# Kernel optimization log

Measured on AMD Instinct MI355X. Metric: run time of the kernel, lower is better.

## Reference

```python
import jax, jax.numpy as jnp
import numpy as np

N = 100000   # num_nodes
E = 1600000  # num_edges
IN, HID, OUT = 128, 128, 64  # in_ft, 2*out_ft, out_ft


def setup_inputs() -> dict:
    key = jax.random.key(0)
    ks = jax.random.split(key, 8)
    x = jax.random.normal(ks[0], (N, IN), dtype=jnp.float32)
    edge_index = jax.random.randint(ks[1], (2, E), 0, N, dtype=jnp.int32)
    # Glorot-style init for GCNConv linear weights
    W1 = jax.random.normal(ks[2], (IN, HID), dtype=jnp.float32) / np.sqrt(IN).astype(np.float32)
    b1 = jnp.zeros((HID,), dtype=jnp.float32)
    W2 = jax.random.normal(ks[3], (HID, OUT), dtype=jnp.float32) / np.sqrt(HID).astype(np.float32)
    b2 = jnp.zeros((OUT,), dtype=jnp.float32)
    a = jnp.array([0.25], dtype=jnp.float32)  # shared PReLU slope (nn.PReLU default)
    return {"x": x, "edge_index": edge_index, "W1": W1, "b1": b1, "W2": W2, "b2": b2, "a": a}


def reference(x, edge_index, W1, b1, W2, b2, a):
    # PyG GCNConv semantics: add self-loops, symmetric normalization
    # norm_e = deg(src)^-1/2 * deg(dst)^-1/2, out[dst] += norm_e * (x @ W)[src] + bias
    src, dst = edge_index[0], edge_index[1]
    loops = jnp.arange(N, dtype=src.dtype)
    s = jnp.concatenate([src, loops])  # [E+N]
    d = jnp.concatenate([dst, loops])  # [E+N]
    deg = jax.ops.segment_sum(jnp.ones_like(d, dtype=x.dtype), d, num_segments=N)
    dis = jax.lax.rsqrt(deg)  # deg >= 1 thanks to self-loops
    norm = (dis[s] * dis[d])[:, None]  # [E+N, 1]

    def gcn_conv(h, W, b):
        hw = h @ W                                   # dense transform [N, F_out]
        msgs = hw[s] * norm                          # gather + scale  [E+N, F_out]
        return jax.ops.segment_sum(msgs, d, num_segments=N) + b  # scatter-add

    prelu = lambda v: jnp.where(v >= 0, v, a * v)

    h = prelu(gcn_conv(x, W1, b1))   # dropout p=0.0 -> identity
    return prelu(gcn_conv(h, W2, b2))
```

## Files before the change

### kernel.cpp

```cpp
#include <hip/hip_runtime.h>

#define N_NODES 100000
#define N_EDGES 1600000
#define BSH 9
#define NB  196
#define EPB 4096
#define CAPSH 14
#define GB  ((N_EDGES + EPB - 1) / EPB)
#define GG  ((N_NODES + 127) / 128)

typedef short bf16x8 __attribute__((ext_vector_type(8)));
typedef float f32x4 __attribute__((ext_vector_type(4)));
typedef float f32x2 __attribute__((ext_vector_type(2)));


__device__ __forceinline__ unsigned pack_bf16x2(float a, float b) {
    unsigned ua = __float_as_uint(a), ub = __float_as_uint(b);
    unsigned ra = (ua + 0x7fffu + ((ua >> 16) & 1u)) >> 16;
    unsigned rb = (ub + 0x7fffu + ((ub >> 16) & 1u)) >> 16;
    return ra | (rb << 16);
}
__device__ __forceinline__ unsigned short bf16_rne(float f) {
    unsigned u = __float_as_uint(f);
    return (unsigned short)((u + 0x7fffu + ((u >> 16) & 1u)) >> 16);
}
__device__ __forceinline__ f32x2 unpk(unsigned u) {
    f32x2 r;
    r.x = __uint_as_float(u << 16);
    r.y = __uint_as_float(u & 0xffff0000u);
    return r;
}


__device__ __forceinline__ void wt_body(const float* W, unsigned short* Wt, int C, int bid) {
    int t = bid * 256 + threadIdx.x;
    if (t >= 128 * C) return;
    int k = t / C, c = t % C;
    int g = k >> 3, j = k & 7;
    Wt[c * 128 + ((g ^ (c & 7)) << 3) + j] = bf16_rne(W[t]);
}

__global__ void setup_k(const float* __restrict__ W1, unsigned short* __restrict__ Wt1,
                        const float* __restrict__ W2, unsigned short* __restrict__ Wt2,
                        int* __restrict__ cursor) {
    int b = blockIdx.x;
    if (b < 64) { wt_body(W1, Wt1, 128, b); }
    else if (b < 96) { wt_body(W2, Wt2, 64, b - 64); }
    else {
        int t = threadIdx.x;
        if (t < NB) cursor[t] = t << CAPSH;
    }
}


__global__ __launch_bounds__(256) void bin_gemm1_k(
        const int* __restrict__ src, const int* __restrict__ dst,
        int* __restrict__ cursor, unsigned* __restrict__ binned,
        const float* __restrict__ X, const unsigned short* __restrict__ Wt,
        unsigned short* __restrict__ Y) {
    __shared__ int lhist[256];
    __shared__ int lcur[256];
    __shared__ short lds_w[128 * 128];
    int tid = threadIdx.x;

    if (blockIdx.x < GB) {
        lhist[tid] = 0;
        __syncthreads();
        int e0 = blockIdx.x * EPB;
#pragma unroll
        for (int i = 0; i < EPB / 256; ++i) {
            int e = e0 + i * 256 + tid;
            if (e < N_EDGES) atomicAdd(&lhist[dst[e] >> BSH], 1);
        }
        __syncthreads();
        {
            int c = lhist[tid];
            lcur[tid] = (tid < NB && c > 0) ? atomicAdd(&cursor[tid], c) : 0;
        }
        __syncthreads();
#pragma unroll
        for (int i = 0; i < EPB / 256; ++i) {
            int e = e0 + i * 256 + tid;
            if (e < N_EDGES) {
                int d = dst[e];
                int b = d >> BSH;
                int pos = atomicAdd(&lcur[b], 1);
                if (pos < ((b + 1) << CAPSH))
                    binned[pos] = ((unsigned)(d & ((1 << BSH) - 1)) << 17) | (unsigned)src[e];
            }
        }
        return;
    }

    {
        const uint4* srcp = (const uint4*)Wt;
        uint4* dstp = (uint4*)lds_w;
        for (int i = tid; i < 128 * 16; i += 256) dstp[i] = srcp[i];
    }
    __syncthreads();
    int lane = tid & 63;
    int r16 = lane & 15, kq = lane >> 4;
    int rbase = (blockIdx.x - GB) * 128 + (tid >> 6) * 32;
    f32x4 acc[2][8] = {};
#pragma unroll
    for (int kk = 0; kk < 4; ++kk) {
        int k0 = kk * 32 + kq * 8;
        bf16x8 a[2];
#pragma unroll
        for (int rt = 0; rt < 2; ++rt) {
            int row = rbase + rt * 16 + r16;
            if (row < N_NODES) {
                const float* xp = X + (size_t)row * 128 + k0;
                float4 f0 = *(const float4*)xp;
                float4 f1 = *(const float4*)(xp + 4);
                uint4 uu = make_uint4(pack_bf16x2(f0.x, f0.y), pack_bf16x2(f0.z, f0.w),
                                      pack_bf16x2(f1.x, f1.y), pack_bf16x2(f1.z, f1.w));
                a[rt] = *(bf16x8*)&uu;
            } else {
                bf16x8 z = {0, 0, 0, 0, 0, 0, 0, 0};
                a[rt] = z;
            }
        }
#pragma unroll
        for (int c = 0; c < 8; ++c) {
            int col = c * 16 + r16;
            int gp = (kk * 4 + kq) ^ (col & 7);
            bf16x8 b = *(const bf16x8*)&lds_w[col * 128 + gp * 8];
            acc[0][c] = __builtin_amdgcn_mfma_f32_16x16x32_bf16(a[0], b, acc[0][c], 0, 0, 0);
            acc[1][c] = __builtin_amdgcn_mfma_f32_16x16x32_bf16(a[1], b, acc[1][c], 0, 0, 0);
        }
    }
#pragma unroll
    for (int rt = 0; rt < 2; ++rt) {
#pragma unroll
        for (int c = 0; c < 8; ++c) {
#pragma unroll
            for (int r = 0; r < 4; ++r) {
                int row = rbase + rt * 16 + kq * 4 + r;
                if (row < N_NODES)
                    Y[(size_t)row * 128 + c * 16 + r16] = bf16_rne(acc[rt][c][r]);
            }
        }
    }
}


__global__ __launch_bounds__(256) void degcsr_k(const unsigned* __restrict__ binned,
                                                const int* __restrict__ cursor,
                                                int2* __restrict__ rowrange,
                                                float* __restrict__ dis,
                                                unsigned* __restrict__ edge, int n) {
    __shared__ int lcnt[1 << BSH];
    __shared__ int ls[256];
    int b = blockIdx.x, tid = threadIdx.x;
    for (int j = tid; j < (1 << BSH); j += 256) lcnt[j] = 0;
    __syncthreads();
    int base = b << CAPSH;
    int total = cursor[b] - base;
    for (int i = tid; i < total; i += 256)
        atomicAdd(&lcnt[binned[base + i] >> 17], 1);
    __syncthreads();
    int v0 = lcnt[2 * tid], v1 = lcnt[2 * tid + 1];
    int sv = v0 + v1;
    ls[tid] = sv;
    __syncthreads();
    for (int off = 1; off < 256; off <<= 1) {
        int t = 0;
        if (tid >= off) t = ls[tid - off];
        __syncthreads();
        ls[tid] += t;
        __syncthreads();
    }
    int pre = ls[tid] - sv;
    int start0 = base + pre;
    int start1 = start0 + v0;
    int nbase = b << BSH;
    int node0 = nbase + 2 * tid, node1 = node0 + 1;
    if (node0 < n) {
        rowrange[node0] = make_int2(start0, start0 + v0);
        dis[node0] = rsqrtf((float)(v0 + 1));
    }
    if (node1 < n) {
        rowrange[node1] = make_int2(start1, start1 + v1);
        dis[node1] = rsqrtf((float)(v1 + 1));
    }
    lcnt[2 * tid] = start0;
    lcnt[2 * tid + 1] = start1;
    __syncthreads();
    for (int i = tid; i < total; i += 256) {
        unsigned u = binned[base + i];
        int pos = atomicAdd(&lcnt[u >> 17], 1);
        edge[pos] = u & 0x1FFFFu;
    }
}


__global__ __launch_bounds__(256) void gemm2_k(const unsigned short* __restrict__ Xv,
                                               const unsigned short* __restrict__ Wt,
                                               unsigned short* __restrict__ Y, int nrows) {
    __shared__ short lds_w[64 * 128];
    int tid = threadIdx.x;
    {
        const uint4* srcp = (const uint4*)Wt;
        uint4* dstp = (uint4*)lds_w;
        for (int i = tid; i < 64 * 16; i += 256) dstp[i] = srcp[i];
    }
    __syncthreads();
    int lane = tid & 63;
    int r16 = lane & 15, kq = lane >> 4;
    int rbase = blockIdx.x * 128 + (tid >> 6) * 32;
    f32x4 acc[2][4] = {};
#pragma unroll
    for (int kk = 0; kk < 4; ++kk) {
        int k0 = kk * 32 + kq * 8;
        bf16x8 a[2];
#pragma unroll
        for (int rt = 0; rt < 2; ++rt) {
            int row = rbase + rt * 16 + r16;
            if (row < nrows) {
                a[rt] = *(const bf16x8*)(Xv + (size_t)row * 128 + k0);
            } else {
                bf16x8 z = {0, 0, 0, 0, 0, 0, 0, 0};
                a[rt] = z;
            }
        }
#pragma unroll
        for (int c = 0; c < 4; ++c) {
            int col = c * 16 + r16;
            int gp = (kk * 4 + kq) ^ (col & 7);
            bf16x8 b = *(const bf16x8*)&lds_w[col * 128 + gp * 8];
            acc[0][c] = __builtin_amdgcn_mfma_f32_16x16x32_bf16(a[0], b, acc[0][c], 0, 0, 0);
            acc[1][c] = __builtin_amdgcn_mfma_f32_16x16x32_bf16(a[1], b, acc[1][c], 0, 0, 0);
        }
    }
#pragma unroll
    for (int rt = 0; rt < 2; ++rt) {
#pragma unroll
        for (int c = 0; c < 4; ++c) {
#pragma unroll
            for (int r = 0; r < 4; ++r) {
                int row = rbase + rt * 16 + kq * 4 + r;
                if (row < nrows)
                    Y[(size_t)row * 64 + c * 16 + r16] = bf16_rne(acc[rt][c][r]);
            }
        }
    }
}


__global__ void agg1_k(const unsigned* __restrict__ hw, const int2* __restrict__ rowrange,
                       const unsigned* __restrict__ edge, const float* __restrict__ dis,
                       const float* __restrict__ bias, const float* __restrict__ aslope,
                       unsigned* __restrict__ out, int n) {
    int w = (blockIdx.x * 256 + threadIdx.x) >> 6;
    int lane = threadIdx.x & 63;
    int g = lane >> 4;
    unsigned li = lane & 15;
    int node = w * 4 + g;
    bool valid = node < n;
    int2 rr = valid ? rowrange[node] : make_int2(0, 0);
    int e0 = rr.x, e1 = rr.y;
    unsigned rowoff = li << 4;
    const char* hwb = (const char*)hw;
    f32x2 acc[4] = {};
    int e = e0;
    while (__any(e < e1)) {
        if (e < e1) {
            unsigned s[4];
            uint4 v[4];
            float wgt[4];
#pragma unroll
            for (int u = 0; u < 4; ++u) {
                int ee = e + u;
                unsigned ec = (unsigned)((ee < e1) ? ee : (e1 - 1));
                s[u] = edge[ec];
            }
#pragma unroll
            for (int u = 0; u < 4; ++u) {
                v[u] = *(const uint4*)(hwb + ((s[u] << 8) | rowoff));
                wgt[u] = dis[s[u]];
            }
#pragma unroll
            for (int u = 0; u < 4; ++u) {
                float nr = (e + u < e1) ? wgt[u] : 0.f;
                f32x2 nr2 = {nr, nr};
                acc[0] += unpk(v[u].x) * nr2;
                acc[1] += unpk(v[u].y) * nr2;
                acc[2] += unpk(v[u].z) * nr2;
                acc[3] += unpk(v[u].w) * nr2;
            }
        }
        e += 4;
    }
    if (valid) {
        float dn = dis[node];
        f32x2 dn2 = {dn, dn};
        uint4 v = *(const uint4*)(hwb + (((unsigned)node << 8) | rowoff));
        acc[0] += unpk(v.x) * dn2;
        acc[1] += unpk(v.y) * dn2;
        acc[2] += unpk(v.z) * dn2;
        acc[3] += unpk(v.w) * dn2;
        float4 b0 = ((const float4*)bias)[li * 2];
        float4 b1 = ((const float4*)bias)[li * 2 + 1];
        float al = aslope[0];
        float r[8] = {dn * acc[0].x + b0.x, dn * acc[0].y + b0.y,
                      dn * acc[1].x + b0.z, dn * acc[1].y + b0.w,
                      dn * acc[2].x + b1.x, dn * acc[2].y + b1.y,
                      dn * acc[3].x + b1.z, dn * acc[3].y + b1.w};
#pragma unroll
        for (int j = 0; j < 8; ++j) r[j] = (r[j] >= 0.f) ? r[j] : al * r[j];
        uint4 o = make_uint4(pack_bf16x2(r[0], r[1]), pack_bf16x2(r[2], r[3]),
                             pack_bf16x2(r[4], r[5]), pack_bf16x2(r[6], r[7]));
        *(uint4*)(out + (size_t)node * 64 + li * 4) = o;
    }
}

__global__ void agg2_k(const unsigned* __restrict__ hw, const int2* __restrict__ rowrange,
                       const unsigned* __restrict__ edge, const float* __restrict__ dis,
                       const float* __restrict__ bias, const float* __restrict__ aslope,
                       float* __restrict__ out, int n) {
    int w = (blockIdx.x * 256 + threadIdx.x) >> 6;
    int lane = threadIdx.x & 63;
    int g = lane >> 4;
    unsigned li = lane & 15;
    int node = w * 4 + g;
    bool valid = node < n;
    int2 rr = valid ? rowrange[node] : make_int2(0, 0);
    int e0 = rr.x, e1 = rr.y;
    unsigned rowoff = li << 3;
    const char* hwb = (const char*)hw;
    f32x2 acc[2] = {};
    int e = e0;
    while (__any(e < e1)) {
        if (e < e1) {
            unsigned s[8];
            uint2 v[8];
            float wgt[8];
#pragma unroll
            for (int u = 0; u < 8; ++u) {
                int ee = e + u;
                unsigned ec = (unsigned)((ee < e1) ? ee : (e1 - 1));
                s[u] = edge[ec];
            }
#pragma unroll
            for (int u = 0; u < 8; ++u) {
                v[u] = *(const uint2*)(hwb + ((s[u] << 7) | rowoff));
                wgt[u] = dis[s[u]];
            }
#pragma unroll
            for (int u = 0; u < 8; ++u) {
                float nr = (e + u < e1) ? wgt[u] : 0.f;
                f32x2 nr2 = {nr, nr};
                acc[0] += unpk(v[u].x) * nr2;
                acc[1] += unpk(v[u].y) * nr2;
            }
        }
        e += 8;
    }
    if (valid) {
        float dn = dis[node];
        f32x2 dn2 = {dn, dn};
        uint2 v = *(const uint2*)(hwb + (((unsigned)node << 7) | rowoff));
        acc[0] += unpk(v.x) * dn2;
        acc[1] += unpk(v.y) * dn2;
        float4 b = ((const float4*)bias)[li];
        float al = aslope[0];
        float r[4] = {dn * acc[0].x + b.x, dn * acc[0].y + b.y,
                      dn * acc[1].x + b.z, dn * acc[1].y + b.w};
#pragma unroll
        for (int j = 0; j < 4; ++j) r[j] = (r[j] >= 0.f) ? r[j] : al * r[j];
        *(float4*)(out + (size_t)node * 64 + li * 4) = make_float4(r[0], r[1], r[2], r[3]);
    }
}


extern "C" void kernel_launch(void* const* d_in, const int* in_sizes, int n_in,
                              void* d_out, int out_size, void* d_ws, size_t ws_size,
                              hipStream_t stream) {
    const float* x  = (const float*)d_in[0];
    const int*   ei = (const int*)d_in[1];
    const int*   src = ei;
    const int*   dst = ei + N_EDGES;
    const float* W1 = (const float*)d_in[2];
    const float* b1 = (const float*)d_in[3];
    const float* W2 = (const float*)d_in[4];
    const float* b2 = (const float*)d_in[5];
    const float* a  = (const float*)d_in[6];
    float* out = (float*)d_out;

    char* ws = (char*)d_ws;
    size_t off = 0;
    auto alloc = [&](size_t bytes) -> void* {
        void* p = ws + off;
        off += (bytes + 255) & ~(size_t)255;
        return p;
    };
    int2*           rowrange  = (int2*)alloc((size_t)N_NODES * 8);
    float*          dis       = (float*)alloc((size_t)N_NODES * 4);
    int*            cursor    = (int*)alloc(NB * 4);
    unsigned*       binned    = (unsigned*)alloc((size_t)NB * (1 << CAPSH) * 4);
    unsigned*       edge      = (unsigned*)alloc((size_t)NB * (1 << CAPSH) * 4);
    unsigned*       hw1       = (unsigned*)alloc((size_t)N_NODES * 64 * 4);
    unsigned*       hbuf      = (unsigned*)alloc((size_t)N_NODES * 64 * 4);
    unsigned*       hw2       = (unsigned*)alloc((size_t)N_NODES * 32 * 4);
    unsigned short* Wt1       = (unsigned short*)alloc(128 * 128 * 2);
    unsigned short* Wt2       = (unsigned short*)alloc(64 * 128 * 2);

    setup_k<<<97, 256, 0, stream>>>(W1, Wt1, W2, Wt2, cursor);
    bin_gemm1_k<<<GB + GG, 256, 0, stream>>>(src, dst, cursor, binned,
                                             x, Wt1, (unsigned short*)hw1);
    degcsr_k<<<NB, 256, 0, stream>>>(binned, cursor, rowrange, dis, edge, N_NODES);

    agg1_k<<<6250, 256, 0, stream>>>(hw1, rowrange, edge, dis, b1, a, hbuf, N_NODES);
    gemm2_k<<<GG, 256, 0, stream>>>((unsigned short*)hbuf, Wt2, (unsigned short*)hw2, N_NODES);
    agg2_k<<<6250, 256, 0, stream>>>(hw2, rowrange, edge, dis, b2, a, out, N_NODES);
}
```

Before: 174.3 us.

## Split aggregation feature columns into halves across paired blocks

Both aggregation kernels now split each node's feature row into two halves, each handled by a separate block, and double the grid. Blocks are interleaved in groups of 8 so that the two halves for the same node groups run close together, presumably so the halves share cached row lines and L2 locality is better. Each thread now gathers half as many bytes per edge, which exposes more parallelism and memory requests in flight. The cost is that the edge indices and dis weights are read twice, once per half.

Measured after the change: 198.8 us. 1.14x slower.

```diff
diff --git a/kernel.cpp b/kernel.cpp
--- a/kernel.cpp
+++ b/kernel.cpp
@@ -8,6 +8,8 @@
 #define CAPSH 14
 #define GB  ((N_EDGES + EPB - 1) / EPB)
 #define GG  ((N_NODES + 127) / 128)
+#define NGRP 6250
+#define AGRID (((NGRP + 3) / 4) * 8)
 
 typedef short bf16x8 __attribute__((ext_vector_type(8)));
 typedef float f32x4 __attribute__((ext_vector_type(4)));
@@ -252,82 +254,19 @@
                        const unsigned* __restrict__ edge, const float* __restrict__ dis,
                        const float* __restrict__ bias, const float* __restrict__ aslope,
                        unsigned* __restrict__ out, int n) {
-    int w = (blockIdx.x * 256 + threadIdx.x) >> 6;
-    int lane = threadIdx.x & 63;
+    int b = blockIdx.x;
+    unsigned half = (b & 7) >> 2;
+    int ng = (b >> 3) * 4 + (b & 3);
+    if (ng >= NGRP) return;
+    int tid = threadIdx.x;
+    int lane = tid & 63;
     int g = lane >> 4;
     unsigned li = lane & 15;
-    int node = w * 4 + g;
+    int node = ng * 16 + (tid >> 6) * 4 + g;
     bool valid = node < n;
     int2 rr = valid ? rowrange[node] : make_int2(0, 0);
     int e0 = rr.x, e1 = rr.y;
-    unsigned rowoff = li << 4;
-    const char* hwb = (const char*)hw;
-    f32x2 acc[4] = {};
-    int e = e0;
-    while (__any(e < e1)) {
-        if (e < e1) {
-            unsigned s[4];
-            uint4 v[4];
-            float wgt[4];
-#pragma unroll
-            for (int u = 0; u < 4; ++u) {
-                int ee = e + u;
-                unsigned ec = (unsigned)((ee < e1) ? ee : (e1 - 1));
-                s[u] = edge[ec];
-            }
-#pragma unroll
-            for (int u = 0; u < 4; ++u) {
-                v[u] = *(const uint4*)(hwb + ((s[u] << 8) | rowoff));
-                wgt[u] = dis[s[u]];
-            }
-#pragma unroll
-            for (int u = 0; u < 4; ++u) {
-                float nr = (e + u < e1) ? wgt[u] : 0.f;
-                f32x2 nr2 = {nr, nr};
-                acc[0] += unpk(v[u].x) * nr2;
-                acc[1] += unpk(v[u].y) * nr2;
-                acc[2] += unpk(v[u].z) * nr2;
-                acc[3] += unpk(v[u].w) * nr2;
-            }
-        }
-        e += 4;
-    }
-    if (valid) {
-        float dn = dis[node];
-        f32x2 dn2 = {dn, dn};
-        uint4 v = *(const uint4*)(hwb + (((unsigned)node << 8) | rowoff));
-        acc[0] += unpk(v.x) * dn2;
-        acc[1] += unpk(v.y) * dn2;
-        acc[2] += unpk(v.z) * dn2;
-        acc[3] += unpk(v.w) * dn2;
-        float4 b0 = ((const float4*)bias)[li * 2];
-        float4 b1 = ((const float4*)bias)[li * 2 + 1];
-        float al = aslope[0];
-        float r[8] = {dn * acc[0].x + b0.x, dn * acc[0].y + b0.y,
-                      dn * acc[1].x + b0.z, dn * acc[1].y + b0.w,
-                      dn * acc[2].x + b1.x, dn * acc[2].y + b1.y,
-                      dn * acc[3].x + b1.z, dn * acc[3].y + b1.w};
-#pragma unroll
-        for (int j = 0; j < 8; ++j) r[j] = (r[j] >= 0.f) ? r[j] : al * r[j];
-        uint4 o = make_uint4(pack_bf16x2(r[0], r[1]), pack_bf16x2(r[2], r[3]),
-                             pack_bf16x2(r[4], r[5]), pack_bf16x2(r[6], r[7]));
-        *(uint4*)(out + (size_t)node * 64 + li * 4) = o;
-    }
-}
-
-__global__ void agg2_k(const unsigned* __restrict__ hw, const int2* __restrict__ rowrange,
-                       const unsigned* __restrict__ edge, const float* __restrict__ dis,
-                       const float* __restrict__ bias, const float* __restrict__ aslope,
-                       float* __restrict__ out, int n) {
-    int w = (blockIdx.x * 256 + threadIdx.x) >> 6;
-    int lane = threadIdx.x & 63;
-    int g = lane >> 4;
-    unsigned li = lane & 15;
-    int node = w * 4 + g;
-    bool valid = node < n;
-    int2 rr = valid ? rowrange[node] : make_int2(0, 0);
-    int e0 = rr.x, e1 = rr.y;
-    unsigned rowoff = li << 3;
+    unsigned rowoff = (half << 7) | (li << 3);
     const char* hwb = (const char*)hw;
     f32x2 acc[2] = {};
     int e = e0;
@@ -344,7 +283,7 @@
             }
 #pragma unroll
             for (int u = 0; u < 8; ++u) {
-                v[u] = *(const uint2*)(hwb + ((s[u] << 7) | rowoff));
+                v[u] = *(const uint2*)(hwb + ((s[u] << 8) | rowoff));
                 wgt[u] = dis[s[u]];
             }
 #pragma unroll
@@ -360,16 +299,76 @@
     if (valid) {
         float dn = dis[node];
         f32x2 dn2 = {dn, dn};
-        uint2 v = *(const uint2*)(hwb + (((unsigned)node << 7) | rowoff));
+        uint2 v = *(const uint2*)(hwb + (((unsigned)node << 8) | rowoff));
         acc[0] += unpk(v.x) * dn2;
         acc[1] += unpk(v.y) * dn2;
-        float4 b = ((const float4*)bias)[li];
+        float4 bb = ((const float4*)bias)[half * 16 + li];
         float al = aslope[0];
-        float r[4] = {dn * acc[0].x + b.x, dn * acc[0].y + b.y,
-                      dn * acc[1].x + b.z, dn * acc[1].y + b.w};
+        float r[4] = {dn * acc[0].x + bb.x, dn * acc[0].y + bb.y,
+                      dn * acc[1].x + bb.z, dn * acc[1].y + bb.w};
 #pragma unroll
         for (int j = 0; j < 4; ++j) r[j] = (r[j] >= 0.f) ? r[j] : al * r[j];
-        *(float4*)(out + (size_t)node * 64 + li * 4) = make_float4(r[0], r[1], r[2], r[3]);
+        uint2 o = make_uint2(pack_bf16x2(r[0], r[1]), pack_bf16x2(r[2], r[3]));
+        *(uint2*)(out + (size_t)node * 64 + half * 32 + li * 2) = o;
+    }
+}
+
+__global__ void agg2_k(const unsigned* __restrict__ hw, const int2* __restrict__ rowrange,
+                       const unsigned* __restrict__ edge, const float* __restrict__ dis,
+                       const float* __restrict__ bias, const float* __restrict__ aslope,
+                       float* __restrict__ out, int n) {
+    int b = blockIdx.x;
+    unsigned half = (b & 7) >> 2;
+    int ng = (b >> 3) * 4 + (b & 3);
+    if (ng >= NGRP) return;
+    int tid = threadIdx.x;
+    int lane = tid & 63;
+    int g = lane >> 4;
+    unsigned li = lane & 15;
+    int node = ng * 16 + (tid >> 6) * 4 + g;
+    bool valid = node < n;
+    int2 rr = valid ? rowrange[node] : make_int2(0, 0);
+    int e0 = rr.x, e1 = rr.y;
+    unsigned rowoff = (half << 6) | (li << 2);
+    const char* hwb = (const char*)hw;
+    f32x2 acc = {};
+    int e = e0;
+    while (__any(e < e1)) {
+        if (e < e1) {
+            unsigned s[8];
+            unsigned v[8];
+            float wgt[8];
+#pragma unroll
+            for (int u = 0; u < 8; ++u) {
+                int ee = e + u;
+                unsigned ec = (unsigned)((ee < e1) ? ee : (e1 - 1));
+                s[u] = edge[ec];
+            }
+#pragma unroll
+            for (int u = 0; u < 8; ++u) {
+                v[u] = *(const unsigned*)(hwb + ((s[u] << 7) | rowoff));
+                wgt[u] = dis[s[u]];
+            }
+#pragma unroll
+            for (int u = 0; u < 8; ++u) {
+                float nr = (e + u < e1) ? wgt[u] : 0.f;
+                f32x2 nr2 = {nr, nr};
+                acc += unpk(v[u]) * nr2;
+            }
+        }
+        e += 8;
+    }
+    if (valid) {
+        float dn = dis[node];
+        f32x2 dn2 = {dn, dn};
+        unsigned v = *(const unsigned*)(hwb + (((unsigned)node << 7) | rowoff));
+        acc += unpk(v) * dn2;
+        float2 bb = ((const float2*)bias)[half * 16 + li];
+        float al = aslope[0];
+        float r[2] = {dn * acc.x + bb.x, dn * acc.y + bb.y};
+#pragma unroll
+        for (int j = 0; j < 2; ++j) r[j] = (r[j] >= 0.f) ? r[j] : al * r[j];
+        *(float2*)(out + (size_t)node * 64 + half * 32 + li * 2) = make_float2(r[0], r[1]);
     }
 }
 
@@ -411,7 +410,7 @@
                                              x, Wt1, (unsigned short*)hw1);
     degcsr_k<<<NB, 256, 0, stream>>>(binned, cursor, rowrange, dis, edge, N_NODES);
 
-    agg1_k<<<6250, 256, 0, stream>>>(hw1, rowrange, edge, dis, b1, a, hbuf, N_NODES);
+    agg1_k<<<AGRID, 256, 0, stream>>>(hw1, rowrange, edge, dis, b1, a, hbuf, N_NODES);
     gemm2_k<<<GG, 256, 0, stream>>>((unsigned short*)hbuf, Wt2, (unsigned short*)hw2, N_NODES);
-    agg2_k<<<6250, 256, 0, stream>>>(hw2, rowrange, edge, dis, b2, a, out, N_NODES);
-}
+    agg2_k<<<AGRID, 256, 0, stream>>>(hw2, rowrange, edge, dis, b2, a, out, N_NODES);
+}
```

## Regroup setup kernels and widen agg2 loads to 16 bytes per lane

Applied to the files above, without the earlier changes.

Folds the weight-transpose work into the binning kernel and fuses the CSR/degree build with the first GEMM into one launch. Cursor initialisation moves to a memset with relative offsets. agg2 now handles 8 nodes per wave with 8 lanes each, loading 16-byte rows and unrolling by 4 edges instead of 8. The aim is to cut a launch and serialisation point and to issue fewer, wider gathers, at the cost of GEMM1 now waiting for binning to finish.

New measurement: 167.7 us (median of 2 runs). 3.8% less time.

```diff
diff --git a/kernel.cpp b/kernel.cpp
--- a/kernel.cpp
+++ b/kernel.cpp
@@ -31,7 +31,6 @@
     return r;
 }
 
-
 __device__ __forceinline__ void wt_body(const float* W, unsigned short* Wt, int C, int bid) {
     int t = bid * 256 + threadIdx.x;
     if (t >= 128 * C) return;
@@ -40,58 +39,105 @@
     Wt[c * 128 + ((g ^ (c & 7)) << 3) + j] = bf16_rne(W[t]);
 }
 
-__global__ void setup_k(const float* __restrict__ W1, unsigned short* __restrict__ Wt1,
-                        const float* __restrict__ W2, unsigned short* __restrict__ Wt2,
-                        int* __restrict__ cursor) {
-    int b = blockIdx.x;
-    if (b < 64) { wt_body(W1, Wt1, 128, b); }
-    else if (b < 96) { wt_body(W2, Wt2, 64, b - 64); }
-    else {
-        int t = threadIdx.x;
-        if (t < NB) cursor[t] = t << CAPSH;
-    }
-}
-
-
-__global__ __launch_bounds__(256) void bin_gemm1_k(
+
+__global__ __launch_bounds__(256) void bin_wt_k(
         const int* __restrict__ src, const int* __restrict__ dst,
         int* __restrict__ cursor, unsigned* __restrict__ binned,
-        const float* __restrict__ X, const unsigned short* __restrict__ Wt,
-        unsigned short* __restrict__ Y) {
+        const float* __restrict__ W1, unsigned short* __restrict__ Wt1,
+        const float* __restrict__ W2, unsigned short* __restrict__ Wt2) {
+    int tid = threadIdx.x;
+    if (blockIdx.x >= GB) {
+        int b2 = blockIdx.x - GB;
+        if (b2 < 64) wt_body(W1, Wt1, 128, b2);
+        else wt_body(W2, Wt2, 64, b2 - 64);
+        return;
+    }
     __shared__ int lhist[256];
     __shared__ int lcur[256];
-    __shared__ short lds_w[128 * 128];
+    lhist[tid] = 0;
+    __syncthreads();
+    int e0 = blockIdx.x * EPB;
+#pragma unroll
+    for (int i = 0; i < EPB / 256; ++i) {
+        int e = e0 + i * 256 + tid;
+        if (e < N_EDGES) atomicAdd(&lhist[dst[e] >> BSH], 1);
+    }
+    __syncthreads();
+    {
+        int c = lhist[tid];
+        lcur[tid] = (tid < NB && c > 0) ? ((tid << CAPSH) + atomicAdd(&cursor[tid], c)) : 0;
+    }
+    __syncthreads();
+#pragma unroll
+    for (int i = 0; i < EPB / 256; ++i) {
+        int e = e0 + i * 256 + tid;
+        if (e < N_EDGES) {
+            int d = dst[e];
+            int b = d >> BSH;
+            int pos = atomicAdd(&lcur[b], 1);
+            if (pos < ((b + 1) << CAPSH))
+                binned[pos] = ((unsigned)(d & ((1 << BSH) - 1)) << 17) | (unsigned)src[e];
+        }
+    }
+}
+
+
+__global__ __launch_bounds__(256) void degcsr_gemm1_k(
+        const unsigned* __restrict__ binned, const int* __restrict__ cursor,
+        int2* __restrict__ rowrange, float* __restrict__ dis,
+        unsigned* __restrict__ edge,
+        const float* __restrict__ X, const unsigned short* __restrict__ Wt,
+        unsigned short* __restrict__ Y, int n) {
+    __shared__ char smem[128 * 128 * 2];
     int tid = threadIdx.x;
 
-    if (blockIdx.x < GB) {
-        lhist[tid] = 0;
+    if (blockIdx.x < NB) {
+        int* lcnt = (int*)smem;
+        int* ls   = (int*)(smem + (1 << BSH) * 4);
+        int b = blockIdx.x;
+        for (int j = tid; j < (1 << BSH); j += 256) lcnt[j] = 0;
         __syncthreads();
-        int e0 = blockIdx.x * EPB;
-#pragma unroll
-        for (int i = 0; i < EPB / 256; ++i) {
-            int e = e0 + i * 256 + tid;
-            if (e < N_EDGES) atomicAdd(&lhist[dst[e] >> BSH], 1);
-        }
+        int base = b << CAPSH;
+        int total = cursor[b];
+        for (int i = tid; i < total; i += 256)
+            atomicAdd(&lcnt[binned[base + i] >> 17], 1);
         __syncthreads();
-        {
-            int c = lhist[tid];
-            lcur[tid] = (tid < NB && c > 0) ? atomicAdd(&cursor[tid], c) : 0;
-        }
+        int v0 = lcnt[2 * tid], v1 = lcnt[2 * tid + 1];
+        int sv = v0 + v1;
+        ls[tid] = sv;
         __syncthreads();
-#pragma unroll
-        for (int i = 0; i < EPB / 256; ++i) {
-            int e = e0 + i * 256 + tid;
-            if (e < N_EDGES) {
-                int d = dst[e];
-                int b = d >> BSH;
-                int pos = atomicAdd(&lcur[b], 1);
-                if (pos < ((b + 1) << CAPSH))
-                    binned[pos] = ((unsigned)(d & ((1 << BSH) - 1)) << 17) | (unsigned)src[e];
-            }
+        for (int off = 1; off < 256; off <<= 1) {
+            int t = 0;
+            if (tid >= off) t = ls[tid - off];
+            __syncthreads();
+            ls[tid] += t;
+            __syncthreads();
+        }
+        int pre = ls[tid] - sv;
+        int start0 = base + pre;
+        int start1 = start0 + v0;
+        int nbase = b << BSH;
+        int node0 = nbase + 2 * tid, node1 = node0 + 1;
+        if (node0 < n) {
+            rowrange[node0] = make_int2(start0, start0 + v0);
+            dis[node0] = rsqrtf((float)(v0 + 1));
+        }
+        if (node1 < n) {
+            rowrange[node1] = make_int2(start1, start1 + v1);
+            dis[node1] = rsqrtf((float)(v1 + 1));
+        }
+        lcnt[2 * tid] = start0;
+        lcnt[2 * tid + 1] = start1;
+        __syncthreads();
+        for (int i = tid; i < total; i += 256) {
+            unsigned u = binned[base + i];
+            int pos = atomicAdd(&lcnt[u >> 17], 1);
+            edge[pos] = u & 0x1FFFFu;
         }
         return;
     }
 
+    short* lds_w = (short*)smem;
     {
         const uint4* srcp = (const uint4*)Wt;
         uint4* dstp = (uint4*)lds_w;
@@ -100,7 +146,7 @@
     __syncthreads();
     int lane = tid & 63;
     int r16 = lane & 15, kq = lane >> 4;
-    int rbase = (blockIdx.x - GB) * 128 + (tid >> 6) * 32;
+    int rbase = (blockIdx.x - NB) * 128 + (tid >> 6) * 32;
     f32x4 acc[2][8] = {};
 #pragma unroll
     for (int kk = 0; kk < 4; ++kk) {
@@ -141,56 +187,6 @@
                     Y[(size_t)row * 128 + c * 16 + r16] = bf16_rne(acc[rt][c][r]);
             }
         }
-    }
-}
-
-
-__global__ __launch_bounds__(256) void degcsr_k(const unsigned* __restrict__ binned,
-                                                const int* __restrict__ cursor,
-                                                int2* __restrict__ rowrange,
-                                                float* __restrict__ dis,
-                                                unsigned* __restrict__ edge, int n) {
-    __shared__ int lcnt[1 << BSH];
-    __shared__ int ls[256];
-    int b = blockIdx.x, tid = threadIdx.x;
-    for (int j = tid; j < (1 << BSH); j += 256) lcnt[j] = 0;
-    __syncthreads();
-    int base = b << CAPSH;
-    int total = cursor[b] - base;
-    for (int i = tid; i < total; i += 256)
-        atomicAdd(&lcnt[binned[base + i] >> 17], 1);
-    __syncthreads();
-    int v0 = lcnt[2 * tid], v1 = lcnt[2 * tid + 1];
-    int sv = v0 + v1;
-    ls[tid] = sv;
-    __syncthreads();
-    for (int off = 1; off < 256; off <<= 1) {
-        int t = 0;
-        if (tid >= off) t = ls[tid - off];
-        __syncthreads();
-        ls[tid] += t;
-        __syncthreads();
-    }
-    int pre = ls[tid] - sv;
-    int start0 = base + pre;
-    int start1 = start0 + v0;
-    int nbase = b << BSH;
-    int node0 = nbase + 2 * tid, node1 = node0 + 1;
-    if (node0 < n) {
-        rowrange[node0] = make_int2(start0, start0 + v0);
-        dis[node0] = rsqrtf((float)(v0 + 1));
-    }
-    if (node1 < n) {
-        rowrange[node1] = make_int2(start1, start1 + v1);
-        dis[node1] = rsqrtf((float)(v1 + 1));
-    }
-    lcnt[2 * tid] = start0;
-    lcnt[2 * tid + 1] = start1;
-    __syncthreads();
-    for (int i = tid; i < total; i += 256) {
-        unsigned u = binned[base + i];
-        int pos = atomicAdd(&lcnt[u >> 17], 1);
-        edge[pos] = u & 0x1FFFFu;
     }
 }
 
@@ -321,55 +317,64 @@
                        float* __restrict__ out, int n) {
     int w = (blockIdx.x * 256 + threadIdx.x) >> 6;
     int lane = threadIdx.x & 63;
-    int g = lane >> 4;
-    unsigned li = lane & 15;
-    int node = w * 4 + g;
+    int g = lane >> 3;
+    unsigned li = lane & 7;
+    int node = w * 8 + g;
     bool valid = node < n;
     int2 rr = valid ? rowrange[node] : make_int2(0, 0);
     int e0 = rr.x, e1 = rr.y;
-    unsigned rowoff = li << 3;
+    unsigned rowoff = li << 4;
     const char* hwb = (const char*)hw;
-    f32x2 acc[2] = {};
+    f32x2 acc[4] = {};
     int e = e0;
     while (__any(e < e1)) {
         if (e < e1) {
-            unsigned s[8];
-            uint2 v[8];
-            float wgt[8];
-#pragma unroll
-            for (int u = 0; u < 8; ++u) {
+            unsigned s[4];
+            uint4 v[4];
+            float wgt[4];
+#pragma unroll
+            for (int u = 0; u < 4; ++u) {
                 int ee = e + u;
                 unsigned ec = (unsigned)((ee < e1) ? ee : (e1 - 1));
                 s[u] = edge[ec];
             }
 #pragma unroll
-            for (int u = 0; u < 8; ++u) {
-                v[u] = *(const uint2*)(hwb + ((s[u] << 7) | rowoff));
+            for (int u = 0; u < 4; ++u) {
+                v[u] = *(const uint4*)(hwb + ((s[u] << 7) | rowoff));
                 wgt[u] = dis[s[u]];
             }
 #pragma unroll
-            for (int u = 0; u < 8; ++u) {
+            for (int u = 0; u < 4; ++u) {
                 float nr = (e + u < e1) ? wgt[u] : 0.f;
                 f32x2 nr2 = {nr, nr};
                 acc[0] += unpk(v[u].x) * nr2;
                 acc[1] += unpk(v[u].y) * nr2;
-            }
-        }
-        e += 8;
+                acc[2] += unpk(v[u].z) * nr2;
+                acc[3] += unpk(v[u].w) * nr2;
+            }
+        }
+        e += 4;
     }
     if (valid) {
         float dn = dis[node];
         f32x2 dn2 = {dn, dn};
-        uint2 v = *(const uint2*)(hwb + (((unsigned)node << 7) | rowoff));
+        uint4 v = *(const uint4*)(hwb + (((unsigned)node << 7) | rowoff));
         acc[0] += unpk(v.x) * dn2;
         acc[1] += unpk(v.y) * dn2;
-        float4 b = ((const float4*)bias)[li];
+        acc[2] += unpk(v.z) * dn2;
+        acc[3] += unpk(v.w) * dn2;
+        float4 b0 = ((const float4*)bias)[li * 2];
+        float4 b1 = ((const float4*)bias)[li * 2 + 1];
         float al = aslope[0];
-        float r[4] = {dn * acc[0].x + b.x, dn * acc[0].y + b.y,
-                      dn * acc[1].x + b.z, dn * acc[1].y + b.w};
-#pragma unroll
-        for (int j = 0; j < 4; ++j) r[j] = (r[j] >= 0.f) ? r[j] : al * r[j];
-        *(float4*)(out + (size_t)node * 64 + li * 4) = make_float4(r[0], r[1], r[2], r[3]);
+        float r[8] = {dn * acc[0].x + b0.x, dn * acc[0].y + b0.y,
+                      dn * acc[1].x + b0.z, dn * acc[1].y + b0.w,
+                      dn * acc[2].x + b1.x, dn * acc[2].y + b1.y,
+                      dn * acc[3].x + b1.z, dn * acc[3].y + b1.w};
+#pragma unroll
+        for (int j = 0; j < 8; ++j) r[j] = (r[j] >= 0.f) ? r[j] : al * r[j];
+        float* op = out + (size_t)node * 64 + li * 8;
+        *(float4*)op = make_float4(r[0], r[1], r[2], r[3]);
+        *(float4*)(op + 4) = make_float4(r[4], r[5], r[6], r[7]);
     }
 }
 
@@ -406,12 +411,12 @@
     unsigned short* Wt1       = (unsigned short*)alloc(128 * 128 * 2);
     unsigned short* Wt2       = (unsigned short*)alloc(64 * 128 * 2);
 
-    setup_k<<<97, 256, 0, stream>>>(W1, Wt1, W2, Wt2, cursor);
-    bin_gemm1_k<<<GB + GG, 256, 0, stream>>>(src, dst, cursor, binned,
-                                             x, Wt1, (unsigned short*)hw1);
-    degcsr_k<<<NB, 256, 0, stream>>>(binned, cursor, rowrange, dis, edge, N_NODES);
-
+    hipMemsetAsync(cursor, 0, NB * 4, stream);
+
+    bin_wt_k<<<GB + 96, 256, 0, stream>>>(src, dst, cursor, binned, W1, Wt1, W2, Wt2);
+    degcsr_gemm1_k<<<NB + GG, 256, 0, stream>>>(binned, cursor, rowrange, dis, edge,
+                                                x, Wt1, (unsigned short*)hw1, N_NODES);
     agg1_k<<<6250, 256, 0, stream>>>(hw1, rowrange, edge, dis, b1, a, hbuf, N_NODES);
     gemm2_k<<<GG, 256, 0, stream>>>((unsigned short*)hbuf, Wt2, (unsigned short*)hw2, N_NODES);
-    agg2_k<<<6250, 256, 0, stream>>>(hw2, rowrange, edge, dis, b2, a, out, N_NODES);
-}
+    agg2_k<<<3125, 256, 0, stream>>>(hw2, rowrange, edge, dis, b2, a, out, N_NODES);
+}
```
